# Kernel tuning notes

Hardware: AMD Instinct MI355X
Metric: run time of the kernel (lower is better)

The kernel has to match this reference:

```python
import jax, jax.numpy as jnp
import numpy as np

NUM_HEADS = 16
HEAD_DIM = 64
SCALE = HEAD_DIM ** (-0.5)


def setup_inputs() -> dict:
    key = jax.random.key(0)
    ks = jax.random.split(key, 7)
    B, T, S, D = 8, 1024, 1500, 1024
    std = 1.0 / np.sqrt(D)
    return {
        "x": jax.random.normal(ks[0], (B, T, D), jnp.float32),
        "k": jax.random.normal(ks[1], (B, S, D), jnp.float32),
        "v": jax.random.normal(ks[2], (B, S, D), jnp.float32),
        "wq": jax.random.normal(ks[3], (D, D), jnp.float32) * std,
        "bq": jnp.zeros((D,), jnp.float32),
        "wo": jax.random.normal(ks[4], (D, D), jnp.float32) * std,
        "bo": jnp.zeros((D,), jnp.float32),
    }


def reference(x, k, v, wq, bq, wo, bo):
    B, T, D = x.shape
    H, Dh = NUM_HEADS, HEAD_DIM
    # q_proj (torch Linear: x @ W^T + b), pre-scaled
    q = (jnp.einsum("btd,ed->bte", x, wq) + bq) * SCALE
    q = q.reshape(B, T, H, Dh)                      # bthd
    kh = k.reshape(B, -1, H, Dh)                    # bshd
    vh = v.reshape(B, -1, H, Dh)
    scores = jnp.einsum("bthd,bshd->bhts", q, kh)   # full [B,H,T,S]
    probs = jax.nn.softmax(scores, axis=-1)
    out = jnp.einsum("bhts,bshd->bthd", probs, vh).reshape(B, T, D)
    return jnp.einsum("btd,ed->bte", out, wo) + bo
```

## Files before the change

### kernel.cpp

```cpp
#include <hip/hip_runtime.h>
#include <hip/hip_bf16.h>

typedef __attribute__((ext_vector_type(8))) short short8;
typedef __attribute__((ext_vector_type(4))) float floatx4;

#define B_ 8
#define T_ 1024
#define S_ 1500
#define SP 1536
#define D_ 1024
#define H_ 16
#define DH 64
#define SCALE2_ 0.1803368801111244f

__device__ __forceinline__ unsigned short f2bf(float f) {
  unsigned u = __float_as_uint(f);
  u += 0x7fffu + ((u >> 16) & 1u);
  return (unsigned short)(u >> 16);
}

__device__ __forceinline__ floatx4 mfma16(short8 a, short8 b, floatx4 c) {
  return __builtin_amdgcn_mfma_f32_16x16x32_bf16(a, b, c, 0, 0, 0);
}

__device__ __forceinline__ void gload_lds16(const unsigned short* g, unsigned short* l) {
  __builtin_amdgcn_global_load_lds(
      (const __attribute__((address_space(1))) unsigned int*)g,
      (__attribute__((address_space(3))) unsigned int*)(unsigned long)(uintptr_t)l, 16, 0, 0);
}

#define N1C (B_ * T_ * D_ / 4)
#define N2C (D_ * D_ / 4)
__global__ void cast3_kernel(const float* __restrict__ x, const float* __restrict__ wq,
                             const float* __restrict__ wo, unsigned short* __restrict__ xb,
                             unsigned short* __restrict__ wqb,
                             unsigned short* __restrict__ wob) {
  int i = blockIdx.x * blockDim.x + threadIdx.x;
  const float* src;
  unsigned short* dst;
  int j;
  if (i < N1C) {
    src = x; dst = xb; j = i;
  } else if (i < N1C + N2C) {
    src = wq; dst = wqb; j = i - N1C;
  } else {
    src = wo; dst = wob; j = i - N1C - N2C;
  }
  float4 v = ((const float4*)src)[j];
  ushort4 o;
  o.x = f2bf(v.x); o.y = f2bf(v.y); o.z = f2bf(v.z); o.w = f2bf(v.w);
  ((ushort4*)dst)[j] = o;
}

__global__ void pack_k_kernel(const float* __restrict__ k,
                              unsigned short* __restrict__ kb) {
  int i = blockIdx.x * blockDim.x + threadIdx.x;
  int dh4 = (i & 15) * 4;
  int j = i >> 4;
  int s = j % SP;
  int bh = j / SP;
  if (bh >= B_ * H_) return;
  int b = bh >> 4, h = bh & 15;
  int p = s & 31;
  int src = (s & ~31) + ((p >> 2) & 3) * 8 + ((p >> 4) & 1) * 4 + (p & 3);
  ushort4 o;
  if (src < S_) {
    float4 v = *(const float4*)(k + (((size_t)(b * S_ + src) * H_ + h) * DH) + dh4);
    o.x = f2bf(v.x); o.y = f2bf(v.y); o.z = f2bf(v.z); o.w = f2bf(v.w);
  } else {
    o = make_ushort4(0, 0, 0, 0);
  }
  *(ushort4*)(kb + ((size_t)bh * SP + s) * DH + dh4) = o;
}

__global__ void pack_vt_kernel(const float* __restrict__ v,
                               unsigned short* __restrict__ vt) {
  __shared__ unsigned short tile[64][72];
  int st = blockIdx.x, bh = blockIdx.y;
  int b = bh >> 4, h = bh & 15;
  int s0 = st * 64;
  int t = threadIdx.x;
  for (int i = t; i < 1024; i += 256) {
    int sl = i >> 4, dh4 = (i & 15) * 4;
    float4 val = make_float4(0.f, 0.f, 0.f, 0.f);
    if (s0 + sl < S_)
      val = *(const float4*)(v + ((size_t)((b * S_ + s0 + sl) * H_ + h)) * DH + dh4);
    tile[dh4 + 0][sl] = f2bf(val.x);
    tile[dh4 + 1][sl] = f2bf(val.y);
    tile[dh4 + 2][sl] = f2bf(val.z);
    tile[dh4 + 3][sl] = f2bf(val.w);
  }
  __syncthreads();
  for (int i = t; i < 1024; i += 256) {
    int d = i >> 4, s4 = (i & 15) * 4;
    ushort4 o;
    o.x = tile[d][s4]; o.y = tile[d][s4 + 1]; o.z = tile[d][s4 + 2]; o.w = tile[d][s4 + 3];
    *(ushort4*)(vt + ((size_t)bh * DH + d) * SP + s0 + s4) = o;
  }
}

#define BK 32
__global__ __launch_bounds__(256, 4) void gemm_bt(const unsigned short* __restrict__ A,
                                                  const unsigned short* __restrict__ Bm,
                                                  const float* __restrict__ bias,
                                                  void* __restrict__ outp, int epi) {
  __shared__ unsigned short As[128 * BK];
  __shared__ unsigned short Bs[128 * BK];
  const int K = 1024;
  int t = threadIdx.x;
  int m0 = blockIdx.y * 128, n0 = blockIdx.x * 128;
  int w = t >> 6, lane = t & 63, quad = lane >> 4, l16 = lane & 15;
  int mw = (w & 1) * 64, nw = (w >> 1) * 64;

  int rloc = lane >> 2, c = lane & 3;
  int g = c ^ (((w * 16 + rloc) >> 1) & 3);
  const unsigned short* pa0 = A + (size_t)(m0 + w * 16 + rloc) * K + g * 8;
  const unsigned short* pa1 = pa0 + (size_t)64 * K;
  const unsigned short* pb0 = Bm + (size_t)(n0 + w * 16 + rloc) * K + g * 8;
  const unsigned short* pb1 = pb0 + (size_t)64 * K;
  unsigned short* lA0 = &As[(w * 16) * BK];
  unsigned short* lA1 = &As[(64 + w * 16) * BK];
  unsigned short* lB0 = &Bs[(w * 16) * BK];
  unsigned short* lB1 = &Bs[(64 + w * 16) * BK];

  floatx4 acc[4][4];
#pragma unroll
  for (int i = 0; i < 4; i++)
#pragma unroll
    for (int j = 0; j < 4; j++) {
      floatx4 z = {0.f, 0.f, 0.f, 0.f};
      acc[i][j] = z;
    }

  int arow = mw + l16;
  int brow = nw + l16;

  for (int kt = 0; kt < K / BK; kt++) {
    __syncthreads();
    gload_lds16(pa0 + kt * BK, lA0);
    gload_lds16(pa1 + kt * BK, lA1);
    gload_lds16(pb0 + kt * BK, lB0);
    gload_lds16(pb1 + kt * BK, lB1);
    __syncthreads();

    short8 af[4], bf[4];
#pragma unroll
    for (int mi = 0; mi < 4; mi++) {
      int r = arow + mi * 16;
      int pc = quad ^ ((r >> 1) & 3);
      af[mi] = *(const short8*)&As[r * BK + pc * 8];
    }
#pragma unroll
    for (int ni = 0; ni < 4; ni++) {
      int r = brow + ni * 16;
      int pc = quad ^ ((r >> 1) & 3);
      bf[ni] = *(const short8*)&Bs[r * BK + pc * 8];
    }
#pragma unroll
    for (int mi = 0; mi < 4; mi++)
#pragma unroll
      for (int ni = 0; ni < 4; ni++)
        acc[mi][ni] = mfma16(af[mi], bf[ni], acc[mi][ni]);
  }

#pragma unroll
  for (int mi = 0; mi < 4; mi++)
#pragma unroll
    for (int ni = 0; ni < 4; ni++) {
      int row = m0 + mw + mi * 16 + quad * 4;
      int col = n0 + nw + ni * 16 + l16;
      float bcol = bias[col];
#pragma unroll
      for (int r = 0; r < 4; r++) {
        float val = acc[mi][ni][r] + bcol;
        int rr = row + r;
        if (epi == 0) {
          int b = rr >> 10, tt = rr & 1023, h = col >> 6, dh = col & 63;
          ((unsigned short*)outp)[(((size_t)(b * 16 + h) * 1024) + tt) * 64 + dh] =
              f2bf(val * SCALE2_);
        } else {
          ((float*)outp)[(size_t)rr * 1024 + col] = val;
        }
      }
    }
}

__global__ __launch_bounds__(512, 4) void attn_kernel(
    const unsigned short* __restrict__ qs, const unsigned short* __restrict__ kb,
    const unsigned short* __restrict__ vt, unsigned short* __restrict__ ob) {
  __shared__ unsigned short Ks[64 * 72];
  __shared__ unsigned short Vs[64 * 72];
  int q = blockIdx.x + (blockIdx.y << 2);
  int ttile = q >> 7, bh = q & 127;
  int b = bh >> 4, h = bh & 15;
  int t = threadIdx.x, w = t >> 6, lane = t & 63, quad = lane >> 4, l16 = lane & 15;

  const unsigned short* qp =
      qs + ((size_t)bh * T_ + ttile * 256 + w * 32 + l16) * DH + quad * 8;
  short8 qa[2][2];
  qa[0][0] = *(const short8*)(qp);
  qa[0][1] = *(const short8*)(qp + 32);
  qa[1][0] = *(const short8*)(qp + 16 * DH);
  qa[1][1] = *(const short8*)(qp + 16 * DH + 32);

  const unsigned short* kbase = kb + (size_t)bh * SP * DH;
  const unsigned short* vbase = vt + (size_t)bh * DH * SP;

  int sr = t >> 3, sc8 = (t & 7) * 8;
  const unsigned short* ksp = kbase + (size_t)sr * DH + sc8;
  const unsigned short* vsp = vbase + (size_t)sr * SP + sc8;
  unsigned short* kl = &Ks[sr * 72 + sc8];
  unsigned short* vl = &Vs[sr * 72 + sc8];

  floatx4 o[2][4];
#pragma unroll
  for (int g = 0; g < 2; g++)
#pragma unroll
    for (int i = 0; i < 4; i++) {
      floatx4 z = {0.f, 0.f, 0.f, 0.f};
      o[g][i] = z;
    }
  float mrow[2] = {-1e30f, -1e30f};
  float lrow[2] = {0.f, 0.f};

  int4 rk = *(const int4*)(ksp);
  int4 rv = *(const int4*)(vsp);

  for (int s0 = 0; s0 < SP; s0 += 64) {
    __syncthreads();
    *(int4*)kl = rk;
    *(int4*)vl = rv;
    __syncthreads();
    if (s0 + 64 < SP) {
      rk = *(const int4*)(ksp + (size_t)(s0 + 64) * DH);
      rv = *(const int4*)(vsp + s0 + 64);
    }

    floatx4 sc[2][4];
#pragma unroll
    for (int nb = 0; nb < 4; nb++) {
      short8 k0 = *(const short8*)&Ks[(nb * 16 + l16) * 72 + quad * 8];
      short8 k1 = *(const short8*)&Ks[(nb * 16 + l16) * 72 + 32 + quad * 8];
      floatx4 a = {0.f, 0.f, 0.f, 0.f};
      a = mfma16(k0, qa[0][0], a);
      a = mfma16(k1, qa[0][1], a);
      sc[0][nb] = a;
      floatx4 a2 = {0.f, 0.f, 0.f, 0.f};
      a2 = mfma16(k0, qa[1][0], a2);
      a2 = mfma16(k1, qa[1][1], a2);
      sc[1][nb] = a2;
    }
    if (s0 + 64 > S_) {
#pragma unroll
      for (int nb = 0; nb < 4; nb++)
#pragma unroll
        for (int r = 0; r < 4; r++) {
          int s_act = s0 + (nb >> 1) * 32 + quad * 8 + (nb & 1) * 4 + r;
          if (s_act >= S_) { sc[0][nb][r] = -1e30f; sc[1][nb][r] = -1e30f; }
        }
    }

#pragma unroll
    for (int g = 0; g < 2; g++) {
      float mx = -1e30f;
#pragma unroll
      for (int nb = 0; nb < 4; nb++) {
        float a0m = fmaxf(sc[g][nb][0], sc[g][nb][1]);
        float a1m = fmaxf(sc[g][nb][2], sc[g][nb][3]);
        mx = fmaxf(mx, fmaxf(a0m, a1m));
      }
      mx = fmaxf(mx, __shfl_xor(mx, 16));
      mx = fmaxf(mx, __shfl_xor(mx, 32));
      float mnew = fmaxf(mrow[g], mx);
      float alpha = exp2f(mrow[g] - mnew);
      mrow[g] = mnew;
      float rs = 0.f;
#pragma unroll
      for (int nb = 0; nb < 4; nb++)
#pragma unroll
        for (int r = 0; r < 4; r++) {
          float p2 = exp2f(sc[g][nb][r] - mnew);
          sc[g][nb][r] = p2;
          rs += p2;
        }
      rs += __shfl_xor(rs, 16);
      rs += __shfl_xor(rs, 32);
      lrow[g] = lrow[g] * alpha + rs;
#pragma unroll
      for (int db = 0; db < 4; db++) {
        o[g][db][0] *= alpha; o[g][db][1] *= alpha;
        o[g][db][2] *= alpha; o[g][db][3] *= alpha;
      }
    }

#pragma unroll
    for (int c = 0; c < 2; c++) {
      union { short8 v; __hip_bfloat162 h[4]; } pk0, pk1;
      pk0.h[0] = __float22bfloat162_rn(make_float2(sc[0][2 * c][0], sc[0][2 * c][1]));
      pk0.h[1] = __float22bfloat162_rn(make_float2(sc[0][2 * c][2], sc[0][2 * c][3]));
      pk0.h[2] = __float22bfloat162_rn(make_float2(sc[0][2 * c + 1][0], sc[0][2 * c + 1][1]));
      pk0.h[3] = __float22bfloat162_rn(make_float2(sc[0][2 * c + 1][2], sc[0][2 * c + 1][3]));
      pk1.h[0] = __float22bfloat162_rn(make_float2(sc[1][2 * c][0], sc[1][2 * c][1]));
      pk1.h[1] = __float22bfloat162_rn(make_float2(sc[1][2 * c][2], sc[1][2 * c][3]));
      pk1.h[2] = __float22bfloat162_rn(make_float2(sc[1][2 * c + 1][0], sc[1][2 * c + 1][1]));
      pk1.h[3] = __float22bfloat162_rn(make_float2(sc[1][2 * c + 1][2], sc[1][2 * c + 1][3]));
#pragma unroll
      for (int db = 0; db < 4; db++) {
        short8 vf = *(const short8*)&Vs[(db * 16 + l16) * 72 + c * 32 + quad * 8];
        o[0][db] = mfma16(vf, pk0.v, o[0][db]);
        o[1][db] = mfma16(vf, pk1.v, o[1][db]);
      }
    }
  }

#pragma unroll
  for (int g = 0; g < 2; g++) {
    float inv = 1.0f / lrow[g];
    int tg = ttile * 256 + w * 32 + g * 16 + l16;
#pragma unroll
    for (int db = 0; db < 4; db++) {
      int dh = db * 16 + quad * 4;
      union { ushort4 s4; __hip_bfloat162 h[2]; } st;
      st.h[0] = __float22bfloat162_rn(make_float2(o[g][db][0] * inv, o[g][db][1] * inv));
      st.h[1] = __float22bfloat162_rn(make_float2(o[g][db][2] * inv, o[g][db][3] * inv));
      *(ushort4*)(ob + ((size_t)(b * T_ + tg) * H_ + h) * DH + dh) = st.s4;
    }
  }
}

extern "C" void kernel_launch(void* const* d_in, const int* in_sizes, int n_in,
                              void* d_out, int out_size, void* d_ws, size_t ws_size,
                              hipStream_t stream) {
  const float* x  = (const float*)d_in[0];
  const float* k  = (const float*)d_in[1];
  const float* v  = (const float*)d_in[2];
  const float* wq = (const float*)d_in[3];
  const float* bq = (const float*)d_in[4];
  const float* wo = (const float*)d_in[5];
  const float* bo = (const float*)d_in[6];
  float* out = (float*)d_out;

  char* ws = (char*)d_ws;
  unsigned short* xb  = (unsigned short*)(ws + 0);
  unsigned short* wqb = (unsigned short*)(ws + 16777216);
  unsigned short* wob = (unsigned short*)(ws + 18874368);
  unsigned short* kbp = (unsigned short*)(ws + 20971520);
  unsigned short* vtp = (unsigned short*)(ws + 46137344);
  unsigned short* qsp = (unsigned short*)(ws + 71303168);
  unsigned short* obp = (unsigned short*)(ws + 88080384);

  {
    int blocks = (N1C + 2 * N2C) / 256;
    cast3_kernel<<<blocks, 256, 0, stream>>>(x, wq, wo, xb, wqb, wob);
  }
  {
    int groups = B_ * H_ * SP * 16;
    pack_k_kernel<<<groups / 256, 256, 0, stream>>>(k, kbp);
    pack_vt_kernel<<<dim3(SP / 64, B_ * H_), 256, 0, stream>>>(v, vtp);
  }
  gemm_bt<<<dim3(D_ / 128, B_ * T_ / 128), 256, 0, stream>>>(xb, wqb, bq, qsp, 0);
  attn_kernel<<<dim3(T_ / 256, B_ * H_), 512, 0, stream>>>(qsp, kbp, vtp, obp);
  gemm_bt<<<dim3(D_ / 128, B_ * T_ / 128), 256, 0, stream>>>(obp, wob, bo, out, 1);
}
```

Before: 340.1 us.

## Double-buffer K/V tiles, shrink attention blocks, and skip rescale below threshold

The attention kernel now uses 256-thread blocks covering 128 query rows and double-buffered K/V shared-memory tiles. The next tile is stored while the current one is consumed, so each iteration needs one barrier instead of two. The online softmax rescales the running max and output only when the new max exceeds the old by more than 8 (in log2 units), which skips most of the alpha multiplies. The cost is twice the shared memory per block and K/V reloaded for twice as many blocks, and the lazy rescale relies on exp2 of up to 8 staying within fp32/bf16 range.

Measured after the change: 328.2 us. 3.5% less time.

```diff
diff --git a/kernel.cpp b/kernel.cpp
--- a/kernel.cpp
+++ b/kernel.cpp
@@ -185,18 +185,19 @@
     }
 }
 
-__global__ __launch_bounds__(512, 4) void attn_kernel(
+#define NT (SP / 64)
+__global__ __launch_bounds__(256, 4) void attn_kernel(
     const unsigned short* __restrict__ qs, const unsigned short* __restrict__ kb,
     const unsigned short* __restrict__ vt, unsigned short* __restrict__ ob) {
-  __shared__ unsigned short Ks[64 * 72];
-  __shared__ unsigned short Vs[64 * 72];
-  int q = blockIdx.x + (blockIdx.y << 2);
-  int ttile = q >> 7, bh = q & 127;
+  __shared__ unsigned short Ks[2][64 * 72];
+  __shared__ unsigned short Vs[2][64 * 72];
+  int p = blockIdx.x + (blockIdx.y << 3);
+  int ttile = p >> 7, bh = p & 127;
   int b = bh >> 4, h = bh & 15;
   int t = threadIdx.x, w = t >> 6, lane = t & 63, quad = lane >> 4, l16 = lane & 15;
 
   const unsigned short* qp =
-      qs + ((size_t)bh * T_ + ttile * 256 + w * 32 + l16) * DH + quad * 8;
+      qs + ((size_t)bh * T_ + ttile * 128 + w * 32 + l16) * DH + quad * 8;
   short8 qa[2][2];
   qa[0][0] = *(const short8*)(qp);
   qa[0][1] = *(const short8*)(qp + 32);
@@ -206,11 +207,13 @@
   const unsigned short* kbase = kb + (size_t)bh * SP * DH;
   const unsigned short* vbase = vt + (size_t)bh * DH * SP;
 
-  int sr = t >> 3, sc8 = (t & 7) * 8;
-  const unsigned short* ksp = kbase + (size_t)sr * DH + sc8;
-  const unsigned short* vsp = vbase + (size_t)sr * SP + sc8;
-  unsigned short* kl = &Ks[sr * 72 + sc8];
-  unsigned short* vl = &Vs[sr * 72 + sc8];
+  int sr = t >> 3, c8 = (t & 7) * 8;
+  const unsigned short* ksp0 = kbase + (size_t)sr * DH + c8;
+  const unsigned short* ksp1 = kbase + (size_t)(sr + 32) * DH + c8;
+  const unsigned short* vsp0 = vbase + (size_t)sr * SP + c8;
+  const unsigned short* vsp1 = vbase + (size_t)(sr + 32) * SP + c8;
+  int klo0 = sr * 72 + c8, klo1 = (sr + 32) * 72 + c8;
+  int vlo0 = sr * 72 + c8, vlo1 = (sr + 32) * 72 + c8;
 
   floatx4 o[2][4];
 #pragma unroll
@@ -223,24 +226,42 @@
   float mrow[2] = {-1e30f, -1e30f};
   float lrow[2] = {0.f, 0.f};
 
-  int4 rk = *(const int4*)(ksp);
-  int4 rv = *(const int4*)(vsp);
-
-  for (int s0 = 0; s0 < SP; s0 += 64) {
+  int4 rk0 = *(const int4*)(ksp0);
+  int4 rk1 = *(const int4*)(ksp1);
+  int4 rv0 = *(const int4*)(vsp0);
+  int4 rv1 = *(const int4*)(vsp1);
+  *(int4*)&Ks[0][klo0] = rk0;
+  *(int4*)&Ks[0][klo1] = rk1;
+  *(int4*)&Vs[0][vlo0] = rv0;
+  *(int4*)&Vs[0][vlo1] = rv1;
+  rk0 = *(const int4*)(ksp0 + (size_t)64 * DH);
+  rk1 = *(const int4*)(ksp1 + (size_t)64 * DH);
+  rv0 = *(const int4*)(vsp0 + 64);
+  rv1 = *(const int4*)(vsp1 + 64);
+
+  for (int n = 0; n < NT; n++) {
+    int s0 = n * 64;
+    int cur = n & 1;
     __syncthreads();
-    *(int4*)kl = rk;
-    *(int4*)vl = rv;
-    __syncthreads();
-    if (s0 + 64 < SP) {
-      rk = *(const int4*)(ksp + (size_t)(s0 + 64) * DH);
-      rv = *(const int4*)(vsp + s0 + 64);
+    if (n + 1 < NT) {
+      *(int4*)&Ks[cur ^ 1][klo0] = rk0;
+      *(int4*)&Ks[cur ^ 1][klo1] = rk1;
+      *(int4*)&Vs[cur ^ 1][vlo0] = rv0;
+      *(int4*)&Vs[cur ^ 1][vlo1] = rv1;
+    }
+    if (n + 2 < NT) {
+      size_t so = (size_t)(s0 + 128);
+      rk0 = *(const int4*)(ksp0 + so * DH);
+      rk1 = *(const int4*)(ksp1 + so * DH);
+      rv0 = *(const int4*)(vsp0 + so);
+      rv1 = *(const int4*)(vsp1 + so);
     }
 
     floatx4 sc[2][4];
 #pragma unroll
     for (int nb = 0; nb < 4; nb++) {
-      short8 k0 = *(const short8*)&Ks[(nb * 16 + l16) * 72 + quad * 8];
-      short8 k1 = *(const short8*)&Ks[(nb * 16 + l16) * 72 + 32 + quad * 8];
+      short8 k0 = *(const short8*)&Ks[cur][(nb * 16 + l16) * 72 + quad * 8];
+      short8 k1 = *(const short8*)&Ks[cur][(nb * 16 + l16) * 72 + 32 + quad * 8];
       floatx4 a = {0.f, 0.f, 0.f, 0.f};
       a = mfma16(k0, qa[0][0], a);
       a = mfma16(k1, qa[0][1], a);
@@ -271,26 +292,30 @@
       }
       mx = fmaxf(mx, __shfl_xor(mx, 16));
       mx = fmaxf(mx, __shfl_xor(mx, 32));
-      float mnew = fmaxf(mrow[g], mx);
-      float alpha = exp2f(mrow[g] - mnew);
-      mrow[g] = mnew;
+      if (__any(mx > mrow[g] + 8.0f)) {
+        float mnew = fmaxf(mrow[g], mx);
+        float alpha = exp2f(mrow[g] - mnew);
+        mrow[g] = mnew;
+        lrow[g] *= alpha;
+#pragma unroll
+        for (int db = 0; db < 4; db++) {
+          o[g][db][0] *= alpha; o[g][db][1] *= alpha;
+          o[g][db][2] *= alpha; o[g][db][3] *= alpha;
+        }
+      }
+      float m = mrow[g];
       float rs = 0.f;
 #pragma unroll
       for (int nb = 0; nb < 4; nb++)
 #pragma unroll
         for (int r = 0; r < 4; r++) {
-          float p2 = exp2f(sc[g][nb][r] - mnew);
+          float p2 = exp2f(sc[g][nb][r] - m);
           sc[g][nb][r] = p2;
           rs += p2;
         }
       rs += __shfl_xor(rs, 16);
       rs += __shfl_xor(rs, 32);
-      lrow[g] = lrow[g] * alpha + rs;
-#pragma unroll
-      for (int db = 0; db < 4; db++) {
-        o[g][db][0] *= alpha; o[g][db][1] *= alpha;
-        o[g][db][2] *= alpha; o[g][db][3] *= alpha;
-      }
+      lrow[g] += rs;
     }
 
 #pragma unroll
@@ -306,7 +331,7 @@
       pk1.h[3] = __float22bfloat162_rn(make_float2(sc[1][2 * c + 1][2], sc[1][2 * c + 1][3]));
 #pragma unroll
       for (int db = 0; db < 4; db++) {
-        short8 vf = *(const short8*)&Vs[(db * 16 + l16) * 72 + c * 32 + quad * 8];
+        short8 vf = *(const short8*)&Vs[cur][(db * 16 + l16) * 72 + c * 32 + quad * 8];
         o[0][db] = mfma16(vf, pk0.v, o[0][db]);
         o[1][db] = mfma16(vf, pk1.v, o[1][db]);
       }
@@ -316,7 +341,7 @@
 #pragma unroll
   for (int g = 0; g < 2; g++) {
     float inv = 1.0f / lrow[g];
-    int tg = ttile * 256 + w * 32 + g * 16 + l16;
+    int tg = ttile * 128 + w * 32 + g * 16 + l16;
 #pragma unroll
     for (int db = 0; db < 4; db++) {
       int dh = db * 16 + quad * 4;
@@ -359,6 +384,6 @@
     pack_vt_kernel<<<dim3(SP / 64, B_ * H_), 256, 0, stream>>>(v, vtp);
   }
   gemm_bt<<<dim3(D_ / 128, B_ * T_ / 128), 256, 0, stream>>>(xb, wqb, bq, qsp, 0);
-  attn_kernel<<<dim3(T_ / 256, B_ * H_), 512, 0, stream>>>(qsp, kbp, vtp, obp);
+  attn_kernel<<<dim3(T_ / 128, B_ * H_), 256, 0, stream>>>(qsp, kbp, vtp, obp);
   gemm_bt<<<dim3(D_ / 128, B_ * T_ / 128), 256, 0, stream>>>(obp, wob, bo, out, 1);
 }
```
